# Performance work log

Measured on AMD Instinct MI355X. Metric: run time of the kernel, lower is better.

Reference implementation:

```python
import jax, jax.numpy as jnp
import numpy as np

B, P, H, N, D, K = 1024, 1024, 4096, 32, 512, 128


def setup_inputs() -> dict:
    key = jax.random.key(0)
    k1, k2, k3, k4, k5 = jax.random.split(key, 5)
    return {
        "proximal_input": jax.random.normal(k1, (B, P), dtype=jnp.float32),
        "distal_input": jax.random.normal(k2, (B, D), dtype=jnp.float32),
        "W": jax.random.normal(k3, (H, P), dtype=jnp.float32) / np.sqrt(P),
        "b": jax.random.normal(k4, (H,), dtype=jnp.float32) / np.sqrt(P),
        "distal": jax.random.normal(k5, (H, N, D), dtype=jnp.float32),
        "k": K,
    }


def reference(proximal_input, distal_input, W, b, distal, k):
    # proximal path: standard linear -> (B, H)
    proximal_output = proximal_input @ W.T + b
    # per-hidden-unit dendrite projections -> (H, B, N)
    distal_output = jnp.einsum('bd,hnd->hbn', distal_input, distal)
    # pick dominant dendrite by absolute value, keep its signed value
    abs_max_idx = jnp.argmax(jnp.abs(distal_output), axis=-1)          # (H, B)
    distal_max = jnp.take_along_axis(
        distal_output, abs_max_idx[..., None], axis=-1)[..., 0].T      # (B, H)
    # sigmoid gate modulates proximal activations
    result = proximal_output * jax.nn.sigmoid(distal_max)              # (B, H)
    # keep only top-k per row (scatter-built 0/1 mask, as in the original)
    _, top_idxs = jax.lax.top_k(result, k)                             # (B, k)
    rows = jnp.arange(result.shape[0])[:, None]
    mask = jnp.zeros_like(result).at[rows, top_idxs].set(1.0)
    return result * mask
```

## Files before the change

### kernel.cpp

```cpp
#include <hip/hip_runtime.h>
#include <cstdint>
#include <cmath>

#define Bsz  1024
#define Pdim 1024
#define Hdim 4096
#define Ndim 32
#define Ddim 512
#define Ktop 128

typedef _Float16 f16x8 __attribute__((ext_vector_type(8)));
typedef float    f32x4 __attribute__((ext_vector_type(4)));

#define GLDS(gsrc, ldst)                                                        \
  __builtin_amdgcn_global_load_lds(                                             \
      (const __attribute__((address_space(1))) unsigned int*)(gsrc),            \
      (__attribute__((address_space(3))) unsigned int*)(ldst), 16, 0, 0)

#define WS_NEEDED 270532608ull

__global__ __launch_bounds__(256) void proximal_gemm(
    const float* __restrict__ pin, const float* __restrict__ W,
    const float* __restrict__ bias, float* __restrict__ out)
{
  __shared__ float Blds[32 * 256];
  __shared__ float Alds[32 * 32];
  const int t  = threadIdx.x;
  const int l  = t & 63;
  const int wv = t >> 6;

  const int ell   = blockIdx.x;
  const int xcd   = ell & 7;
  const int q     = ell >> 3;
  const int htile = xcd * 2 + (q >> 5);
  const int btile = q & 31;
  const int h0 = htile * 256, b0 = btile * 32;

  float acc[8][4];
#pragma unroll
  for (int i = 0; i < 8; i++)
    for (int j = 0; j < 4; j++) acc[i][j] = 0.f;

  const float* wrow = W + (size_t)(h0 + t) * Pdim;
  const int ab = t >> 3, ak = (t & 7) * 4;
  const float* arow = pin + (size_t)(b0 + ab) * Pdim + ak;

  for (int kt = 0; kt < Pdim / 32; ++kt) {
    const int p0 = kt * 32;
    float wbuf[32];
#pragma unroll
    for (int f = 0; f < 8; f++) {
      float4 v = *(const float4*)(wrow + p0 + f * 4);
      wbuf[f * 4 + 0] = v.x; wbuf[f * 4 + 1] = v.y;
      wbuf[f * 4 + 2] = v.z; wbuf[f * 4 + 3] = v.w;
    }
    float4 av = *(const float4*)(arow + p0);
    __syncthreads();
#pragma unroll
    for (int f = 0; f < 32; f++) Blds[f * 256 + t] = wbuf[f];
    Alds[(ak + 0) * 32 + ab] = av.x;
    Alds[(ak + 1) * 32 + ab] = av.y;
    Alds[(ak + 2) * 32 + ab] = av.z;
    Alds[(ak + 3) * 32 + ab] = av.w;
    __syncthreads();
#pragma unroll
    for (int k = 0; k < 32; k++) {
      float4 bv  = *(const float4*)&Blds[k * 256 + 4 * l];
      float4 alo = *(const float4*)&Alds[k * 32 + 8 * wv];
      float4 ahi = *(const float4*)&Alds[k * 32 + 8 * wv + 4];
      float a0[8] = {alo.x, alo.y, alo.z, alo.w, ahi.x, ahi.y, ahi.z, ahi.w};
#pragma unroll
      for (int i = 0; i < 8; i++) {
        acc[i][0] += a0[i] * bv.x;
        acc[i][1] += a0[i] * bv.y;
        acc[i][2] += a0[i] * bv.z;
        acc[i][3] += a0[i] * bv.w;
      }
    }
  }
  float4 bb = *(const float4*)(bias + h0 + 4 * l);
#pragma unroll
  for (int i = 0; i < 8; i++) {
    float4 o;
    o.x = acc[i][0] + bb.x;
    o.y = acc[i][1] + bb.y;
    o.z = acc[i][2] + bb.z;
    o.w = acc[i][3] + bb.w;
    *(float4*)(out + (size_t)(b0 + 8 * wv + i) * Hdim + h0 + 4 * l) = o;
  }
}

__global__ __launch_bounds__(256) void convert_distal(
    const float* __restrict__ src, char* __restrict__ dstA)
{
  const int gid = blockIdx.x * 256 + threadIdx.x;
  const int np_ = gid >> 6;
  const int e   = (gid & 63) * 8;
  float4 v0 = *(const float4*)(src + (size_t)np_ * Ddim + e);
  float4 v1 = *(const float4*)(src + (size_t)np_ * Ddim + e + 4);
  const int ntile = np_ >> 7, r = np_ & 127, ks = e >> 5, k = e & 31;
  char* base = dstA + (size_t)(ntile * 16 + ks) * 16384;
  const int off = r * 64 + (((k >> 3) * 16) ^ ((r & 3) << 4));
  const float f[8] = {v0.x, v0.y, v0.z, v0.w, v1.x, v1.y, v1.z, v1.w};
  f16x8 hi, lo;
#pragma unroll
  for (int j = 0; j < 8; j++) {
    const _Float16 h = (_Float16)f[j];
    hi[j] = h;
    lo[j] = (_Float16)((f[j] - (float)h) * 256.f);
  }
  *(f16x8*)(base + off)        = hi;
  *(f16x8*)(base + 8192 + off) = lo;
}

__global__ __launch_bounds__(256) void convert_din(
    const float* __restrict__ src, char* __restrict__ dstB)
{
  const int gid = blockIdx.x * 256 + threadIdx.x;
  const int b   = gid >> 6;
  const int e   = (gid & 63) * 8;
  float4 v0 = *(const float4*)(src + (size_t)b * Ddim + e);
  float4 v1 = *(const float4*)(src + (size_t)b * Ddim + e + 4);
  const int btile = b >> 7, c = b & 127, ks = e >> 5, k = e & 31;
  char* base = dstB + (size_t)(btile * 16 + ks) * 16384;
  const int off = c * 64 + (((k >> 3) * 16) ^ ((c & 3) << 4));
  const float f[8] = {v0.x, v0.y, v0.z, v0.w, v1.x, v1.y, v1.z, v1.w};
  f16x8 hi, lo;
#pragma unroll
  for (int j = 0; j < 8; j++) {
    const _Float16 h = (_Float16)f[j];
    hi[j] = h;
    lo[j] = (_Float16)((f[j] - (float)h) * 256.f);
  }
  *(f16x8*)(base + off)        = hi;
  *(f16x8*)(base + 8192 + off) = lo;
}

__global__ __launch_bounds__(256, 2) void distal_mfma(
    const char* __restrict__ Aw, const char* __restrict__ Bw,
    float* __restrict__ out)
{
  __shared__ _Float16 lds[16384];
  const int t = threadIdx.x, lane = t & 63, wv = t >> 6;
  const int g = lane >> 4, c15 = lane & 15;
  const int wrow0 = (wv >> 1) * 64, wcol0 = (wv & 1) * 64;

  const int blk = blockIdx.x;
  const int xcd = blk & 7, q = blk >> 3;
  const int ntile = xcd * 128 + (q >> 3);
  const int btile = q & 7;

  f32x4 acc[4][4], accx[4][4];
#pragma unroll
  for (int mi = 0; mi < 4; mi++)
#pragma unroll
    for (int ni = 0; ni < 4; ni++) {
      acc[mi][ni]  = (f32x4){0.f, 0.f, 0.f, 0.f};
      accx[mi][ni] = (f32x4){0.f, 0.f, 0.f, 0.f};
    }

  const char* Abase = Aw + (size_t)(ntile * 16) * 16384;
  const char* Bbase = Bw + (size_t)(btile * 16) * 16384;

  for (int ks = 0; ks < 16; ++ks) {
    const char* As = Abase + ks * 16384;
    const char* Bs = Bbase + ks * 16384;
#pragma unroll
    for (int j = 0; j < 4; j++) {
      const int ch = j * 4 + wv;
      GLDS(As + ch * 1024 + lane * 16, (char*)lds + ch * 1024);
      GLDS(Bs + ch * 1024 + lane * 16, (char*)lds + 16384 + ch * 1024);
    }
    __syncthreads();

    f16x8 ah[4], al[4], bh[4], bl[4];
#pragma unroll
    for (int mi = 0; mi < 4; mi++) {
      const int r   = wrow0 + mi * 16 + c15;
      const int off = r * 64 + ((g * 16) ^ ((r & 3) << 4));
      ah[mi] = *(const f16x8*)((const char*)lds + off);
      al[mi] = *(const f16x8*)((const char*)lds + 8192 + off);
    }
#pragma unroll
    for (int ni = 0; ni < 4; ni++) {
      const int c   = wcol0 + ni * 16 + c15;
      const int off = c * 64 + ((g * 16) ^ ((c & 3) << 4));
      bh[ni] = *(const f16x8*)((const char*)lds + 16384 + off);
      bl[ni] = *(const f16x8*)((const char*)lds + 24576 + off);
    }
#pragma unroll
    for (int mi = 0; mi < 4; mi++)
#pragma unroll
      for (int ni = 0; ni < 4; ni++) {
        acc[mi][ni]  = __builtin_amdgcn_mfma_f32_16x16x32_f16(ah[mi], bh[ni], acc[mi][ni],  0, 0, 0);
        accx[mi][ni] = __builtin_amdgcn_mfma_f32_16x16x32_f16(ah[mi], bl[ni], accx[mi][ni], 0, 0, 0);
        accx[mi][ni] = __builtin_amdgcn_mfma_f32_16x16x32_f16(al[mi], bh[ni], accx[mi][ni], 0, 0, 0);
      }
    __syncthreads();
  }

#pragma unroll
  for (int hh = 0; hh < 2; ++hh) {
#pragma unroll
    for (int ni = 0; ni < 4; ++ni) {
      float bestA = -1.f, bestV = 0.f;
      int   bestN = 999;
#pragma unroll
      for (int m2 = 0; m2 < 2; ++m2) {
        const int mi = hh * 2 + m2;
#pragma unroll
        for (int reg = 0; reg < 4; ++reg) {
          const float v = acc[mi][ni][reg] + accx[mi][ni][reg] * 0.00390625f;
          const float a = fabsf(v);
          const int   n = m2 * 16 + g * 4 + reg;
          if (a > bestA) { bestA = a; bestV = v; bestN = n; }
        }
      }
#pragma unroll
      for (int m = 16; m <= 32; m <<= 1) {
        const float oa = __shfl_xor(bestA, m, 64);
        const float ov = __shfl_xor(bestV, m, 64);
        const int   on = __shfl_xor(bestN, m, 64);
        if (oa > bestA || (oa == bestA && on < bestN)) {
          bestA = oa; bestV = ov; bestN = on;
        }
      }
      if (g == 0) {
        const int bcol = btile * 128 + wcol0 + ni * 16 + c15;
        const int h    = ntile * 4 + (wv >> 1) * 2 + hh;
        const float gate = 1.f / (1.f + expf(-bestV));
        out[(size_t)bcol * Hdim + h] *= gate;
      }
    }
  }
}

__global__ __launch_bounds__(256) void distal_gate_fb(
    const float* __restrict__ din, const float* __restrict__ distal,
    float* __restrict__ out)
{
  __shared__ float Blds[32 * 256];
  __shared__ float Alds[32 * 32];
  const int t  = threadIdx.x;
  const int l  = t & 63;
  const int wv = t >> 6;
  const int ell   = blockIdx.x;
  const int xcd   = ell & 7;
  const int q     = ell >> 3;
  const int htile = xcd * 64 + (q >> 5);
  const int btile = q & 31;
  const int n0 = htile * 256, b0 = btile * 32;

  float acc[8][4];
#pragma unroll
  for (int i = 0; i < 8; i++)
    for (int j = 0; j < 4; j++) acc[i][j] = 0.f;

  const float* brow = distal + (size_t)(n0 + t) * Ddim;
  const int ab = t >> 3, ak = (t & 7) * 4;
  const float* arow = din + (size_t)(b0 + ab) * Ddim + ak;

  for (int kt = 0; kt < Ddim / 32; ++kt) {
    const int d0 = kt * 32;
    float wbuf[32];
#pragma unroll
    for (int f = 0; f < 8; f++) {
      float4 v = *(const float4*)(brow + d0 + f * 4);
      wbuf[f * 4 + 0] = v.x; wbuf[f * 4 + 1] = v.y;
      wbuf[f * 4 + 2] = v.z; wbuf[f * 4 + 3] = v.w;
    }
    float4 av = *(const float4*)(arow + d0);
    __syncthreads();
#pragma unroll
    for (int f = 0; f < 32; f++) Blds[f * 256 + t] = wbuf[f];
    Alds[(ak + 0) * 32 + ab] = av.x;
    Alds[(ak + 1) * 32 + ab] = av.y;
    Alds[(ak + 2) * 32 + ab] = av.z;
    Alds[(ak + 3) * 32 + ab] = av.w;
    __syncthreads();
#pragma unroll
    for (int k = 0; k < 32; k++) {
      float4 bv  = *(const float4*)&Blds[k * 256 + 4 * l];
      float4 alo = *(const float4*)&Alds[k * 32 + 8 * wv];
      float4 ahi = *(const float4*)&Alds[k * 32 + 8 * wv + 4];
      float a0[8] = {alo.x, alo.y, alo.z, alo.w, ahi.x, ahi.y, ahi.z, ahi.w};
#pragma unroll
      for (int i = 0; i < 8; i++) {
        acc[i][0] += a0[i] * bv.x;
        acc[i][1] += a0[i] * bv.y;
        acc[i][2] += a0[i] * bv.z;
        acc[i][3] += a0[i] * bv.w;
      }
    }
  }
  const int i0  = l & 7;
  const int grp = l >> 3;
  float v = 0.f;
#pragma unroll
  for (int bi = 0; bi < 8; bi++) {
    float bav = fabsf(acc[bi][0]);
    float bv_ = acc[bi][0];
    int   bn  = 4 * i0;
#pragma unroll
    for (int j = 1; j < 4; j++) {
      float av2 = fabsf(acc[bi][j]);
      if (av2 > bav) { bav = av2; bv_ = acc[bi][j]; bn = 4 * i0 + j; }
    }
#pragma unroll
    for (int m = 1; m < 8; m <<= 1) {
      float oav = __shfl_xor(bav, m, 64);
      float ov  = __shfl_xor(bv_, m, 64);
      int   on  = __shfl_xor(bn,  m, 64);
      if (oav > bav || (oav == bav && on < bn)) { bav = oav; bv_ = ov; bn = on; }
    }
    if (bi == i0) v = bv_;
  }
  const float gate = 1.f / (1.f + expf(-v));
  const size_t idx = (size_t)(b0 + 8 * wv + i0) * Hdim + (size_t)htile * 8 + grp;
  out[idx] *= gate;
}

__device__ __forceinline__ unsigned keyf(float f) {
  unsigned u = __float_as_uint(f);
  return (u & 0x80000000u) ? ~u : (u | 0x80000000u);
}

__global__ __launch_bounds__(256) void topk_mask(float* __restrict__ out)
{
  __shared__ float vals[Hdim];
  __shared__ unsigned hist[256];
  __shared__ unsigned sc[4];
  __shared__ unsigned s_prefix, s_kk;
  const int t = threadIdx.x;
  float* row = out + (size_t)blockIdx.x * Hdim;

#pragma unroll
  for (int qq = 0; qq < 4; qq++) {
    float4 v = *(const float4*)(row + qq * 1024 + t * 4);
    *(float4*)&vals[qq * 1024 + t * 4] = v;
  }
  if (t == 0) { s_prefix = 0u; s_kk = Ktop; }
  __syncthreads();

  for (int shift = 24; shift >= 0; shift -= 8) {
    hist[t] = 0u;
    __syncthreads();
    const unsigned prefix = s_prefix;
    const unsigned maskhi = (shift == 24) ? 0u : (0xFFFFFFFFu << (shift + 8));
    for (int c = 0; c < 16; c++) {
      unsigned u = keyf(vals[c * 256 + t]);
      if ((u & maskhi) == prefix)
        atomicAdd(&hist[(u >> shift) & 255u], 1u);
    }
    __syncthreads();
    if (t == 0) {
      unsigned kk = s_kk, cum = 0;
      int bin = 255;
      for (; bin > 0; --bin) {
        unsigned c = hist[bin];
        if (cum + c >= kk) break;
        cum += c;
      }
      s_kk = kk - cum;
      s_prefix = prefix | ((unsigned)bin << shift);
    }
    __syncthreads();
  }
  const unsigned T  = s_prefix;
  const unsigned kk = s_kk;

  const int lane = t & 63, w = t >> 6;
  unsigned running = 0;
  for (int c = 0; c < 16; c++) {
    const int h = c * 256 + t;
    const float v = vals[h];
    const unsigned u = keyf(v);
    const bool tie = (u == T);
    unsigned long long m = __ballot(tie);
    unsigned lpfx = (unsigned)__popcll(m & ((1ull << lane) - 1ull));
    if (lane == 0) sc[w] = (unsigned)__popcll(m);
    __syncthreads();
    unsigned off = 0;
#pragma unroll
    for (int ww = 0; ww < 4; ww++) if (ww < w) off += sc[ww];
    const unsigned rank = running + off + lpfx;
    row[h] = (u > T) ? v : ((tie && rank < kk) ? v : 0.f);
    const unsigned tot = sc[0] + sc[1] + sc[2] + sc[3];
    __syncthreads();
    running += tot;
  }
}

extern "C" void kernel_launch(void* const* d_in, const int* in_sizes, int n_in,
                              void* d_out, int out_size, void* d_ws, size_t ws_size,
                              hipStream_t stream)
{
  (void)in_sizes; (void)n_in; (void)out_size;
  const float* pin  = (const float*)d_in[0];
  const float* dinp = (const float*)d_in[1];
  const float* W    = (const float*)d_in[2];
  const float* bias = (const float*)d_in[3];
  const float* dst  = (const float*)d_in[4];
  float* out = (float*)d_out;

  hipLaunchKernelGGL(proximal_gemm, dim3(512), dim3(256), 0, stream, pin, W, bias, out);

  if (ws_size >= WS_NEEDED) {
    char* Aw = (char*)d_ws;
    char* Bw = (char*)d_ws + 268435456ull;
    hipLaunchKernelGGL(convert_distal, dim3(32768), dim3(256), 0, stream, dst,  Aw);
    hipLaunchKernelGGL(convert_din,    dim3(256),   dim3(256), 0, stream, dinp, Bw);
    hipLaunchKernelGGL(distal_mfma,    dim3(8192),  dim3(256), 0, stream, Aw, Bw, out);
  } else {
    hipLaunchKernelGGL(distal_gate_fb, dim3(16384), dim3(256), 0, stream, dinp, dst, out);
  }

  hipLaunchKernelGGL(topk_mask, dim3(Bsz), dim3(256), 0, stream, out);
}
```

Before: 717.9 us.

## Double-buffer distal MFMA LDS staging and pre-swizzle fragments into lane order

```diff
diff --git a/kernel.cpp b/kernel.cpp
--- a/kernel.cpp
+++ b/kernel.cpp
@@ -100,7 +100,7 @@
   float4 v1 = *(const float4*)(src + (size_t)np_ * Ddim + e + 4);
   const int ntile = np_ >> 7, r = np_ & 127, ks = e >> 5, k = e & 31;
   char* base = dstA + (size_t)(ntile * 16 + ks) * 16384;
-  const int off = r * 64 + (((k >> 3) * 16) ^ ((r & 3) << 4));
+  const int off = (r >> 4) * 1024 + (((k >> 3) * 16 + (r & 15)) * 16);
   const float f[8] = {v0.x, v0.y, v0.z, v0.w, v1.x, v1.y, v1.z, v1.w};
   f16x8 hi, lo;
 #pragma unroll
@@ -123,7 +123,7 @@
   float4 v1 = *(const float4*)(src + (size_t)b * Ddim + e + 4);
   const int btile = b >> 7, c = b & 127, ks = e >> 5, k = e & 31;
   char* base = dstB + (size_t)(btile * 16 + ks) * 16384;
-  const int off = c * 64 + (((k >> 3) * 16) ^ ((c & 3) << 4));
+  const int off = (c >> 4) * 1024 + (((k >> 3) * 16 + (c & 15)) * 16);
   const float f[8] = {v0.x, v0.y, v0.z, v0.w, v1.x, v1.y, v1.z, v1.w};
   f16x8 hi, lo;
 #pragma unroll
@@ -140,7 +140,7 @@
     const char* __restrict__ Aw, const char* __restrict__ Bw,
     float* __restrict__ out)
 {
-  __shared__ _Float16 lds[16384];
+  __shared__ __align__(16) char lds[2][32768];
   const int t = threadIdx.x, lane = t & 63, wv = t >> 6;
   const int g = lane >> 4, c15 = lane & 15;
   const int wrow0 = (wv >> 1) * 64, wcol0 = (wv & 1) * 64;
@@ -162,31 +162,37 @@
   const char* Abase = Aw + (size_t)(ntile * 16) * 16384;
   const char* Bbase = Bw + (size_t)(btile * 16) * 16384;
 
-  for (int ks = 0; ks < 16; ++ks) {
+  auto STAGE = [&](char* bufp, int ks) {
     const char* As = Abase + ks * 16384;
     const char* Bs = Bbase + ks * 16384;
 #pragma unroll
     for (int j = 0; j < 4; j++) {
       const int ch = j * 4 + wv;
-      GLDS(As + ch * 1024 + lane * 16, (char*)lds + ch * 1024);
-      GLDS(Bs + ch * 1024 + lane * 16, (char*)lds + 16384 + ch * 1024);
-    }
-    __syncthreads();
-
+      GLDS(As + ch * 1024 + lane * 16, bufp + ch * 1024);
+      GLDS(Bs + ch * 1024 + lane * 16, bufp + 16384 + ch * 1024);
+    }
+  };
+
+  STAGE(lds[0], 0);
+  __syncthreads();
+
+  int cur = 0;
+  for (int ks = 0; ks < 16; ++ks) {
+    if (ks < 15) STAGE(lds[cur ^ 1], ks + 1);
+
+    const char* L = lds[cur];
     f16x8 ah[4], al[4], bh[4], bl[4];
 #pragma unroll
     for (int mi = 0; mi < 4; mi++) {
-      const int r   = wrow0 + mi * 16 + c15;
-      const int off = r * 64 + ((g * 16) ^ ((r & 3) << 4));
-      ah[mi] = *(const f16x8*)((const char*)lds + off);
-      al[mi] = *(const f16x8*)((const char*)lds + 8192 + off);
+      const int f = (wv >> 1) * 4 + mi;
+      ah[mi] = *(const f16x8*)(L + f * 1024 + lane * 16);
+      al[mi] = *(const f16x8*)(L + 8192 + f * 1024 + lane * 16);
     }
 #pragma unroll
     for (int ni = 0; ni < 4; ni++) {
-      const int c   = wcol0 + ni * 16 + c15;
-      const int off = c * 64 + ((g * 16) ^ ((c & 3) << 4));
-      bh[ni] = *(const f16x8*)((const char*)lds + 16384 + off);
-      bl[ni] = *(const f16x8*)((const char*)lds + 24576 + off);
+      const int f = (wv & 1) * 4 + ni;
+      bh[ni] = *(const f16x8*)(L + 16384 + f * 1024 + lane * 16);
+      bl[ni] = *(const f16x8*)(L + 24576 + f * 1024 + lane * 16);
     }
 #pragma unroll
     for (int mi = 0; mi < 4; mi++)
@@ -196,7 +202,9 @@
         accx[mi][ni] = __builtin_amdgcn_mfma_f32_16x16x32_f16(ah[mi], bl[ni], accx[mi][ni], 0, 0, 0);
         accx[mi][ni] = __builtin_amdgcn_mfma_f32_16x16x32_f16(al[mi], bh[ni], accx[mi][ni], 0, 0, 0);
       }
-    __syncthreads();
+
+    __syncthreads();
+    cur ^= 1;
   }
 
 #pragma unroll
```

New measurement: 699.3 us. 1.03x faster.
